# Kernel optimization log

Hardware: AMD Instinct MI355X
Metric: run time of the kernel (lower is better)

Reference implementation:

```python
import jax, jax.numpy as jnp
import numpy as np

N = 50000      # num_nodes
E = 800000     # num_edges
F = 29         # num_node_features
IN = F + 3     # in_channels after hstack with pos
H = 64         # hidden_dim
B = 50         # batch_size (num graphs)
L = 7          # num GINConv layers


def setup_inputs() -> dict:
    key = jax.random.key(0)
    ks = jax.random.split(key, 12)
    s_in = 1.0 / np.sqrt(IN)
    s_h = 1.0 / np.sqrt(H)
    return {
        "x": jax.random.normal(ks[0], (N, F), jnp.float32),
        "pos": jax.random.normal(ks[1], (N, 3), jnp.float32),
        "edge_index": jax.random.randint(ks[2], (2, E), 0, N),
        "batch": jnp.sort(jax.random.randint(ks[3], (N,), 0, B)),
        # GINConv l: MLP = Linear(in,H) -> ReLU -> Linear(H,H)
        "W1_first": jax.random.normal(ks[4], (IN, H), jnp.float32) * s_in,
        "W1_rest": jax.random.normal(ks[5], (L - 1, H, H), jnp.float32) * s_h,
        "b1": jax.random.normal(ks[6], (L, H), jnp.float32) * 0.01,
        "W2": jax.random.normal(ks[7], (L, H, H), jnp.float32) * s_h,
        "b2": jax.random.normal(ks[8], (L, H), jnp.float32) * 0.01,
        "lin_w": jax.random.normal(ks[9], (H, 1), jnp.float32) * s_h,
        "lin_b": jax.random.normal(ks[10], (1,), jnp.float32) * 0.01,
    }


def reference(x, pos, edge_index, batch, W1_first, W1_rest, b1, W2, b2, lin_w, lin_b):
    src, dst = edge_index[0], edge_index[1]
    h = jnp.concatenate([x, pos], axis=1)  # [N, IN]

    def gin_conv(h, Wa, ba, Wb, bb):
        # sum aggregation of source features at destination nodes, eps=0
        agg = jax.ops.segment_sum(h[src], dst, num_segments=N)
        z = h + agg
        z = jax.nn.relu(z @ Wa + ba)
        return z @ Wb + bb

    h = jax.nn.relu(gin_conv(h, W1_first, b1[0], W2[0], b2[0]))
    for l in range(1, L):
        h = gin_conv(h, W1_rest[l - 1], b1[l], W2[l], b2[l])
        if l < L - 1:  # no activation after last conv (jk=None)
            h = jax.nn.relu(h)

    # global mean pool per graph
    sums = jax.ops.segment_sum(h, batch, num_segments=B)            # [B, H]
    counts = jax.ops.segment_sum(jnp.ones((N,), h.dtype), batch, num_segments=B)
    pooled = sums / jnp.maximum(counts, 1.0)[:, None]

    return pooled @ lin_w + lin_b  # [B, 1]
```

## Files before the change

### kernel.cpp

```cpp
#include <hip/hip_runtime.h>
#include <stdint.h>

#define NF 29
#define HD 64
#define NL 7
#define LDW 72
#define NCHUNK 256
#define BSH 8
#define PER_M (64 * LDW)
#define TILE 32

typedef __attribute__((ext_vector_type(8))) __bf16 bf16x8;
typedef __attribute__((ext_vector_type(4))) float floatx4;
typedef int int32x4 __attribute__((ext_vector_type(4)));
typedef float f32x4v __attribute__((ext_vector_type(4)));

extern "C" __device__ f32x4v llvm_amdgcn_raw_buffer_load_fp32x4(
    int32x4 srsrc, int voffset, int soffset, int cachepolicy)
    __asm("llvm.amdgcn.raw.buffer.load.v4f32");

__device__ __forceinline__ int32x4 make_srd(const void* p) {
    unsigned long long a = (unsigned long long)p;
    int32x4 r;
    r.x = (int)(a & 0xFFFFFFFFull);
    r.y = (int)(a >> 32);
    r.z = -1;
    r.w = 0x00020000;
    return r;
}
__device__ __forceinline__ uint4 bload16_sc0(int32x4 srd, int voff) {
    f32x4v v = llvm_amdgcn_raw_buffer_load_fp32x4(srd, voff, 0, 1 );
    union { f32x4v f; uint4 u; } c;
    c.f = v;
    return c.u;
}

__device__ __forceinline__ unsigned short f2bf(float x) {
    unsigned u = __float_as_uint(x);
    unsigned r = (u + 0x7fffu + ((u >> 16) & 1u)) >> 16;
    return (unsigned short)r;
}
__device__ __forceinline__ unsigned pack_bf2(float x, float y) {
    return (unsigned)f2bf(x) | ((unsigned)f2bf(y) << 16);
}
__device__ __forceinline__ float bflo(uint32_t u) { return __uint_as_float(u << 16); }
__device__ __forceinline__ float bfhi(uint32_t u) { return __uint_as_float(u & 0xffff0000u); }
__device__ __forceinline__ float bf2f(unsigned short s) {
    return __uint_as_float((uint32_t)s << 16);
}

__global__ void front_kernel(const float* __restrict__ x, const float* __restrict__ pos,
                             unsigned short* __restrict__ h0,
                             const float* __restrict__ W1f, const float* __restrict__ W1r,
                             const float* __restrict__ W2, unsigned short* __restrict__ wpk,
                             const int* __restrict__ dst, int E, int chunk,
                             int* __restrict__ bcnt, int* __restrict__ bsum,
                             float* __restrict__ pool, int N, int B) {
    __shared__ int hist[256];
    const int H0B = (N * 4 + 255) / 256;
    const int WPB = (NL * 2 * PER_M + 255) / 256;
    int blk = blockIdx.x;
    if (blk < H0B) {
        int t = blk * 256 + threadIdx.x;
        if (t < N * 4) {
            int n = t >> 2, q = t & 3;
            const float* xr = x + (size_t)n * NF;
            float f[8];
            if (q < 3) {
                #pragma unroll
                for (int i = 0; i < 8; ++i) f[i] = xr[q * 8 + i];
            } else {
                #pragma unroll
                for (int i = 0; i < 5; ++i) f[i] = xr[24 + i];
                f[5] = pos[n * 3 + 0]; f[6] = pos[n * 3 + 1]; f[7] = pos[n * 3 + 2];
            }
            uint4 pk;
            pk.x = pack_bf2(f[0], f[1]); pk.y = pack_bf2(f[2], f[3]);
            pk.z = pack_bf2(f[4], f[5]); pk.w = pack_bf2(f[6], f[7]);
            ((uint4*)h0)[t] = pk;
        }
    } else if (blk < H0B + WPB) {
        int bw = blk - H0B;
        if (bw == 0) {
            for (int i = threadIdx.x; i < B * HD; i += 256) pool[i] = 0.f;
        }
        int t = bw * 256 + threadIdx.x;
        if (t < NL * 2 * PER_M) {
            int l = t / (2 * PER_M);
            int r = t - l * 2 * PER_M;
            int m = r / PER_M;
            int q = r - m * PER_M;
            int j = q / LDW, k = q - j * LDW;
            float v = 0.f;
            if (m == 0) {
                int ind = (l == 0) ? 32 : 64;
                if (k < ind) v = (l == 0) ? W1f[k * 64 + j]
                                          : W1r[(size_t)(l - 1) * 4096 + (size_t)k * 64 + j];
            } else {
                if (k < 64) v = W2[(size_t)l * 4096 + (size_t)k * 64 + j];
            }
            wpk[t] = f2bf(v);
        }
    } else {
        int c = blk - H0B - WPB;
        int tid = threadIdx.x;
        hist[tid] = 0;
        __syncthreads();
        int lo = c * chunk, hi = min(E, lo + chunk);
        for (int e = lo + tid; e < hi; e += 256) atomicAdd(&hist[dst[e] >> BSH], 1);
        __syncthreads();
        bcnt[c * 256 + tid] = hist[tid];
        if (hist[tid]) atomicAdd(&bsum[tid], hist[tid]);
    }
}

__global__ void bucket_off_kernel(const int* __restrict__ bcnt, const int* __restrict__ bsum,
                                  int* __restrict__ boffT) {
    __shared__ int red[256];
    __shared__ int s[256];
    int b = blockIdx.x, t = threadIdx.x;
    red[t] = (t < b) ? bsum[t] : 0;
    int c = bcnt[t * 256 + b];
    __syncthreads();
    #pragma unroll
    for (int off = 128; off > 0; off >>= 1) {
        if (t < off) red[t] += red[t + off];
        __syncthreads();
    }
    int bstart_b = red[0];
    s[t] = c;
    __syncthreads();
    for (int off = 1; off < 256; off <<= 1) {
        int v = (t >= off) ? s[t - off] : 0;
        __syncthreads();
        s[t] += v;
        __syncthreads();
    }
    int excl = s[t] - c;
    boffT[t * 256 + b] = bstart_b + excl;
}

__global__ void bucket_scatter_kernel(const int* __restrict__ src, const int* __restrict__ dst,
                                      int E, int chunk, const int* __restrict__ boffT,
                                      unsigned int* __restrict__ ebuf) {
    __shared__ int cur[256];
    int tid = threadIdx.x, c = blockIdx.x;
    cur[tid] = boffT[c * 256 + tid];
    __syncthreads();
    int lo = c * chunk, hi = min(E, lo + chunk);
    for (int e = lo + tid; e < hi; e += 256) {
        int d = dst[e];
        int p = atomicAdd(&cur[d >> BSH], 1);
        ebuf[p] = (unsigned int)src[e] | ((unsigned int)(d & 255) << 16);
    }
}

__global__ void final_scatter_kernel(const unsigned int* __restrict__ ebuf,
                                     const int* __restrict__ bsum,
                                     int* __restrict__ rowptr,
                                     unsigned short* __restrict__ colsrc, int N, int E) {
    __shared__ int red[256];
    __shared__ int cnt[256];
    __shared__ int cur[256];
    __shared__ int s[256];
    int b = blockIdx.x, t = threadIdx.x;
    red[t] = (t < b) ? bsum[t] : 0;
    cnt[t] = 0;
    __syncthreads();
    #pragma unroll
    for (int off = 128; off > 0; off >>= 1) {
        if (t < off) red[t] += red[t + off];
        __syncthreads();
    }
    int lo = red[0];
    int hi = lo + bsum[b];
    if (b == 0 && t == 0) rowptr[N] = E;
    for (int e = lo + t; e < hi; e += 256) atomicAdd(&cnt[ebuf[e] >> 16], 1);
    __syncthreads();
    int c = cnt[t];
    s[t] = c;
    __syncthreads();
    for (int off = 1; off < 256; off <<= 1) {
        int v = (t >= off) ? s[t - off] : 0;
        __syncthreads();
        s[t] += v;
        __syncthreads();
    }
    int base = lo + s[t] - c;
    int node = (b << BSH) + t;
    if (node < N) rowptr[node] = base;
    cur[t] = base;
    __syncthreads();
    for (int e = lo + t; e < hi; e += 256) {
        unsigned int ed = ebuf[e];
        int p = atomicAdd(&cur[ed >> 16], 1);
        colsrc[p] = (unsigned short)(ed & 0xffffu);
    }
}

template<int IND, bool RELU_OUT, bool LAST>
__global__ __launch_bounds__(256, 8)
void gin_layer_kernel(const unsigned short* __restrict__ hin,
                      const int* __restrict__ rowptr, const unsigned short* __restrict__ colsrc,
                      const unsigned short* __restrict__ wAT, const unsigned short* __restrict__ wBT,
                      const float* __restrict__ ba, const float* __restrict__ bb,
                      unsigned short* __restrict__ hout,
                      const int* __restrict__ batch, float* __restrict__ pool,
                      int N)
{
    __shared__ __align__(16) unsigned short zbuf[TILE * LDW];
    __shared__ __align__(16) unsigned short t1buf[TILE * LDW];

    const int tid = threadIdx.x;
    const int lane = tid & 63;
    const int w = tid >> 6;
    const int tile0 = blockIdx.x * TILE;

    const int32x4 srd = make_srd(hin);
    const int g = lane >> 3;
    const int j = lane & 7;
    const int node = tile0 + w * 8 + g;

    int rp;
    {
        int idx = tile0 + w * 8 + (lane < 9 ? lane : 8);
        if (idx > N) idx = N;
        rp = rowptr[idx];
    }
    int e0 = __shfl(rp, g);
    int e1 = __shfl(rp, g + 1);
    if (node >= N) { e0 = 0; e1 = 0; }

    float acc[8] = {0.f, 0.f, 0.f, 0.f, 0.f, 0.f, 0.f, 0.f};
    auto addrow = [&](uint4 u) {
        acc[0] += bflo(u.x); acc[1] += bfhi(u.x);
        acc[2] += bflo(u.y); acc[3] += bfhi(u.y);
        acc[4] += bflo(u.z); acc[5] += bfhi(u.z);
        acc[6] += bflo(u.w); acc[7] += bfhi(u.w);
    };

    if constexpr (IND == 64) {
        const int f4 = lane & 7;
        if (node < N) addrow(bload16_sc0(srd, node * 128 + f4 * 16));
        int e = e0;
        int idxv = (e + j < e1) ? (int)colsrc[e + j] : 0;
        for (; e + 7 < e1; e += 8) {
            int en = e + 8;
            int idx_next = (en + j < e1) ? (int)colsrc[en + j] : 0;
            int s[8];
            #pragma unroll
            for (int q = 0; q < 8; ++q) s[q] = __shfl(idxv, g * 8 + q);
            uint4 u[8];
            #pragma unroll
            for (int q = 0; q < 8; ++q) u[q] = bload16_sc0(srd, s[q] * 128 + f4 * 16);
            #pragma unroll
            for (int q = 0; q < 8; ++q) addrow(u[q]);
            idxv = idx_next;
        }
        {
            int rem = e1 - e;
            #pragma unroll
            for (int q = 0; q < 8; ++q) {
                if (q < rem) {
                    int s = __shfl(idxv, g * 8 + q);
                    addrow(bload16_sc0(srd, s * 128 + f4 * 16));
                }
            }
        }
        uint4 pk;
        pk.x = pack_bf2(acc[0], acc[1]); pk.y = pack_bf2(acc[2], acc[3]);
        pk.z = pack_bf2(acc[4], acc[5]); pk.w = pack_bf2(acc[6], acc[7]);
        *(uint4*)&zbuf[(w * 8 + g) * LDW + f4 * 8] = pk;
    } else {
        const int p = (lane >> 2) & 1;
        const int f4 = lane & 3;
        if (node < N && p == 0) addrow(bload16_sc0(srd, node * 64 + f4 * 16));
        int e = e0 + p;
        for (; e + 7 < e1; e += 8) {
            int s0 = colsrc[e], s1 = colsrc[e + 2], s2 = colsrc[e + 4], s3 = colsrc[e + 6];
            uint4 u0 = bload16_sc0(srd, s0 * 64 + f4 * 16);
            uint4 u1 = bload16_sc0(srd, s1 * 64 + f4 * 16);
            uint4 u2 = bload16_sc0(srd, s2 * 64 + f4 * 16);
            uint4 u3 = bload16_sc0(srd, s3 * 64 + f4 * 16);
            addrow(u0); addrow(u1); addrow(u2); addrow(u3);
        }
        while (e < e1) { addrow(bload16_sc0(srd, (int)colsrc[e] * 64 + f4 * 16)); e += 2; }
        #pragma unroll
        for (int i = 0; i < 8; ++i) acc[i] += __shfl_xor(acc[i], 4);
        if (p == 0) {
            uint4 pk;
            pk.x = pack_bf2(acc[0], acc[1]); pk.y = pack_bf2(acc[2], acc[3]);
            pk.z = pack_bf2(acc[4], acc[5]); pk.w = pack_bf2(acc[6], acc[7]);
            *(uint4*)&zbuf[(w * 8 + g) * LDW + f4 * 8] = pk;
        }
    }
    __syncthreads();

    const int n0 = lane & 15, quad = lane >> 4;
    const int stripe = w & 1, jhalf = w >> 1;
    const int row0 = stripe * 16;
    const int jt0 = jhalf * 2, jt1 = jhalf * 2 + 1;

    floatx4 c0, c1;
    {
        float b0v = ba[jt0 * 16 + n0], b1v = ba[jt1 * 16 + n0];
        c0 = (floatx4){b0v, b0v, b0v, b0v};
        c1 = (floatx4){b1v, b1v, b1v, b1v};
    }
    #pragma unroll
    for (int kk = 0; kk < IND / 32; ++kk) {
        bf16x8 a   = *(const bf16x8*)&zbuf[(row0 + n0) * LDW + kk * 32 + quad * 8];
        bf16x8 br0 = *(const bf16x8*)&wAT[(jt0 * 16 + n0) * LDW + kk * 32 + quad * 8];
        bf16x8 br1 = *(const bf16x8*)&wAT[(jt1 * 16 + n0) * LDW + kk * 32 + quad * 8];
        c0 = __builtin_amdgcn_mfma_f32_16x16x32_bf16(a, br0, c0, 0, 0, 0);
        c1 = __builtin_amdgcn_mfma_f32_16x16x32_bf16(a, br1, c1, 0, 0, 0);
    }
    #pragma unroll
    for (int r = 0; r < 4; ++r) {
        int row = row0 + quad * 4 + r;
        t1buf[row * LDW + jt0 * 16 + n0] = f2bf(fmaxf(c0[r], 0.f));
        t1buf[row * LDW + jt1 * 16 + n0] = f2bf(fmaxf(c1[r], 0.f));
    }
    __syncthreads();

    {
        float b0v = bb[jt0 * 16 + n0], b1v = bb[jt1 * 16 + n0];
        c0 = (floatx4){b0v, b0v, b0v, b0v};
        c1 = (floatx4){b1v, b1v, b1v, b1v};
    }
    #pragma unroll
    for (int kk = 0; kk < 2; ++kk) {
        bf16x8 a   = *(const bf16x8*)&t1buf[(row0 + n0) * LDW + kk * 32 + quad * 8];
        bf16x8 br0 = *(const bf16x8*)&wBT[(jt0 * 16 + n0) * LDW + kk * 32 + quad * 8];
        bf16x8 br1 = *(const bf16x8*)&wBT[(jt1 * 16 + n0) * LDW + kk * 32 + quad * 8];
        c0 = __builtin_amdgcn_mfma_f32_16x16x32_bf16(a, br0, c0, 0, 0, 0);
        c1 = __builtin_amdgcn_mfma_f32_16x16x32_bf16(a, br1, c1, 0, 0, 0);
    }
    #pragma unroll
    for (int r = 0; r < 4; ++r) {
        int row = row0 + quad * 4 + r;
        float v0 = c0[r], v1 = c1[r];
        if (RELU_OUT) { v0 = fmaxf(v0, 0.f); v1 = fmaxf(v1, 0.f); }
        zbuf[row * LDW + jt0 * 16 + n0] = f2bf(v0);
        zbuf[row * LDW + jt1 * 16 + n0] = f2bf(v1);
    }
    __syncthreads();

    if constexpr (!LAST) {
        int nl = tid >> 3, c4 = tid & 7;
        int nodeo = tile0 + nl;
        if (nodeo < N) {
            uint4 v = *(const uint4*)&zbuf[nl * LDW + c4 * 8];
            ((uint4*)hout)[(size_t)nodeo * 8 + c4] = v;
        }
    } else {
        int nl0 = w * 8;
        int bvec = 0;
        if (lane < 8) {
            int idx = tile0 + nl0 + lane;
            bvec = batch[idx < N ? idx : (N - 1)];
        }
        int bsel = -1;
        float run = 0.f;
        for (int i = 0; i < 8; ++i) {
            int nodeo = tile0 + nl0 + i;
            if (nodeo >= N) break;
            int b = __shfl(bvec, i);
            float v = bf2f(zbuf[(nl0 + i) * LDW + lane]);
            if (b != bsel) {
                if (bsel >= 0) atomicAdd(&pool[bsel * HD + lane], run);
                bsel = b; run = 0.f;
            }
            run += v;
        }
        if (bsel >= 0) atomicAdd(&pool[bsel * HD + lane], run);
    }
}

__global__ void final_kernel(const float* __restrict__ pool, const int* __restrict__ batch,
                             const float* __restrict__ lin_w, const float* __restrict__ lin_b,
                             float* __restrict__ out, int B, int N) {
    int b = blockIdx.x;
    int lane = threadIdx.x;
    int lo = 0, hi = N;
    while (lo < hi) { int m = (lo + hi) >> 1; if (batch[m] < b) lo = m + 1; else hi = m; }
    int lb = lo;
    lo = 0; hi = N;
    while (lo < hi) { int m = (lo + hi) >> 1; if (batch[m] <= b) lo = m + 1; else hi = m; }
    float c = fmaxf((float)(lo - lb), 1.f);
    float v = pool[b * HD + lane] / c * lin_w[lane];
    for (int off = 32; off > 0; off >>= 1) v += __shfl_down(v, off);
    if (lane == 0) out[b] = v + lin_b[0];
}

extern "C" void kernel_launch(void* const* d_in, const int* in_sizes, int n_in,
                              void* d_out, int out_size, void* d_ws, size_t ws_size,
                              hipStream_t stream)
{
    const float* x   = (const float*)d_in[0];
    const float* pos = (const float*)d_in[1];
    const int*  eidx = (const int*)d_in[2];
    const int* batch = (const int*)d_in[3];
    const float* W1f = (const float*)d_in[4];
    const float* W1r = (const float*)d_in[5];
    const float* b1  = (const float*)d_in[6];
    const float* W2  = (const float*)d_in[7];
    const float* b2  = (const float*)d_in[8];
    const float* lw  = (const float*)d_in[9];
    const float* lb  = (const float*)d_in[10];

    int N = in_sizes[3];
    int E = in_sizes[2] / 2;
    int B = out_size;
    const int* src = eidx;
    const int* dst = eidx + E;

    char* ws = (char*)d_ws;
    size_t off = 0;
    auto alloc = [&](size_t bytes) -> void* {
        void* p = ws + off;
        off += (bytes + 255) & ~(size_t)255;
        return p;
    };
    unsigned short* bufA = (unsigned short*)alloc((size_t)N * HD * 2);
    unsigned short* bufB = (unsigned short*)alloc((size_t)N * HD * 2);
    int*   rowptr = (int*)  alloc((size_t)(N + 1) * 4);
    unsigned short* colsrc = (unsigned short*)alloc((size_t)E * 2);
    unsigned int* ebuf = (unsigned int*)alloc((size_t)E * 4);
    float* pool   = (float*)alloc((size_t)B * HD * 4);
    int*   bcnt   = (int*)  alloc((size_t)NCHUNK * 256 * 4);
    int*   boffT  = (int*)  alloc((size_t)NCHUNK * 256 * 4);
    int*   bsum   = (int*)  alloc(256 * 4);
    unsigned short* wpk = (unsigned short*)alloc((size_t)NL * 2 * PER_M * 2);

    hipMemsetAsync(bsum, 0, 256 * 4, stream);

    int nbuk = (N + 255) >> BSH;
    int chunk = (E + NCHUNK - 1) / NCHUNK;

    const int H0B = (N * 4 + 255) / 256;
    const int WPB = (NL * 2 * PER_M + 255) / 256;
    front_kernel<<<H0B + WPB + NCHUNK, 256, 0, stream>>>(
        x, pos, bufA, W1f, W1r, W2, wpk, dst, E, chunk, bcnt, bsum, pool, N, B);
    bucket_off_kernel<<<nbuk, 256, 0, stream>>>(bcnt, bsum, boffT);
    bucket_scatter_kernel<<<NCHUNK, 256, 0, stream>>>(src, dst, E, chunk, boffT, ebuf);
    final_scatter_kernel<<<nbuk, 256, 0, stream>>>(ebuf, bsum, rowptr, colsrc, N, E);

    const int gblocks = (N + TILE - 1) / TILE;
    gin_layer_kernel<32, true, false><<<gblocks, 256, 0, stream>>>(
        bufA, rowptr, colsrc, wpk + 0 * PER_M, wpk + 1 * PER_M, b1, b2, bufB,
        nullptr, nullptr, N);
    unsigned short* cur_in = bufB;
    unsigned short* cur_out = bufA;
    for (int l = 1; l < NL; ++l) {
        const unsigned short* wa = wpk + (size_t)(2 * l + 0) * PER_M;
        const unsigned short* wb = wpk + (size_t)(2 * l + 1) * PER_M;
        const float* ba = b1 + l * HD;
        const float* bb = b2 + l * HD;
        if (l < NL - 1) {
            gin_layer_kernel<HD, true, false><<<gblocks, 256, 0, stream>>>(
                cur_in, rowptr, colsrc, wa, wb, ba, bb, cur_out, nullptr, nullptr, N);
            unsigned short* tmp = cur_in; cur_in = cur_out; cur_out = tmp;
        } else {
            gin_layer_kernel<HD, false, true><<<gblocks, 256, 0, stream>>>(
                cur_in, rowptr, colsrc, wa, wb, ba, bb, nullptr, batch, pool, N);
        }
    }
    final_kernel<<<B, 64, 0, stream>>>(pool, batch, lw, lb, (float*)d_out, B, N);
}
```

Baseline: 240.1 us.

## Add 16-node-tile GIN layer kernel with 16 lanes per node for hidden layers

Adds a new kernel for the 64-wide hidden layers that processes 16 nodes per block instead of 32. Each node's edges are gathered by 16 lanes split into two edge-parity halves, which are combined with a shuffle. The MLP runs as a single 16x16 MFMA tile per wave. The aim is to double the number of blocks and the memory-level parallelism for the irregular neighbour gather, which should hide latency better. In exchange, the weight loads and block overhead are paid once per 16 nodes instead of per 32, and part of the MFMA work is wasted on a smaller tile.

```diff
diff --git a/kernel.cpp b/kernel.cpp
--- a/kernel.cpp
+++ b/kernel.cpp
@@ -218,7 +218,6 @@
 
     const int32x4 srd = make_srd(hin);
     const int g = lane >> 3;
-    const int j = lane & 7;
     const int node = tile0 + w * 8 + g;
 
     int rp;
@@ -239,39 +238,7 @@
         acc[6] += bflo(u.w); acc[7] += bfhi(u.w);
     };
 
-    if constexpr (IND == 64) {
-        const int f4 = lane & 7;
-        if (node < N) addrow(bload16_sc0(srd, node * 128 + f4 * 16));
-        int e = e0;
-        int idxv = (e + j < e1) ? (int)colsrc[e + j] : 0;
-        for (; e + 7 < e1; e += 8) {
-            int en = e + 8;
-            int idx_next = (en + j < e1) ? (int)colsrc[en + j] : 0;
-            int s[8];
-            #pragma unroll
-            for (int q = 0; q < 8; ++q) s[q] = __shfl(idxv, g * 8 + q);
-            uint4 u[8];
-            #pragma unroll
-            for (int q = 0; q < 8; ++q) u[q] = bload16_sc0(srd, s[q] * 128 + f4 * 16);
-            #pragma unroll
-            for (int q = 0; q < 8; ++q) addrow(u[q]);
-            idxv = idx_next;
-        }
-        {
-            int rem = e1 - e;
-            #pragma unroll
-            for (int q = 0; q < 8; ++q) {
-                if (q < rem) {
-                    int s = __shfl(idxv, g * 8 + q);
-                    addrow(bload16_sc0(srd, s * 128 + f4 * 16));
-                }
-            }
-        }
-        uint4 pk;
-        pk.x = pack_bf2(acc[0], acc[1]); pk.y = pack_bf2(acc[2], acc[3]);
-        pk.z = pack_bf2(acc[4], acc[5]); pk.w = pack_bf2(acc[6], acc[7]);
-        *(uint4*)&zbuf[(w * 8 + g) * LDW + f4 * 8] = pk;
-    } else {
+    {
         const int p = (lane >> 2) & 1;
         const int f4 = lane & 3;
         if (node < N && p == 0) addrow(bload16_sc0(srd, node * 64 + f4 * 16));
@@ -374,6 +341,153 @@
             run += v;
         }
         if (bsel >= 0) atomicAdd(&pool[bsel * HD + lane], run);
+    }
+}
+
+template<bool RELU_OUT, bool LAST>
+__global__ __launch_bounds__(256, 8)
+void gin_layer16_kernel(const unsigned short* __restrict__ hin,
+                        const int* __restrict__ rowptr, const unsigned short* __restrict__ colsrc,
+                        const unsigned short* __restrict__ wAT, const unsigned short* __restrict__ wBT,
+                        const float* __restrict__ ba, const float* __restrict__ bb,
+                        unsigned short* __restrict__ hout,
+                        const int* __restrict__ batch, float* __restrict__ pool,
+                        int N)
+{
+    __shared__ __align__(16) unsigned short zbuf[16 * LDW];
+    __shared__ __align__(16) unsigned short t1buf[16 * LDW];
+
+    const int tid = threadIdx.x;
+    const int lane = tid & 63;
+    const int w = tid >> 6;
+    const int tile0 = blockIdx.x * 16;
+
+    const int32x4 srd = make_srd(hin);
+    const int g = lane >> 4;
+    const int u = lane & 15;
+    const int p = u >> 3;
+    const int f4 = u & 7;
+    const int node = tile0 + w * 4 + g;
+
+    int rp;
+    {
+        int idx = tile0 + w * 4 + (lane < 5 ? lane : 4);
+        if (idx > N) idx = N;
+        rp = rowptr[idx];
+    }
+    int e0 = __shfl(rp, g);
+    int e1 = __shfl(rp, g + 1);
+    if (node >= N) { e0 = 0; e1 = 0; }
+
+    float acc[8] = {0.f, 0.f, 0.f, 0.f, 0.f, 0.f, 0.f, 0.f};
+    auto addrow = [&](uint4 uu) {
+        acc[0] += bflo(uu.x); acc[1] += bfhi(uu.x);
+        acc[2] += bflo(uu.y); acc[3] += bfhi(uu.y);
+        acc[4] += bflo(uu.z); acc[5] += bfhi(uu.z);
+        acc[6] += bflo(uu.w); acc[7] += bfhi(uu.w);
+    };
+
+    if (node < N && p == 0) addrow(bload16_sc0(srd, node * 128 + f4 * 16));
+
+    int eb = e0;
+    int idxv = (eb + u < e1) ? (int)colsrc[eb + u] : 0;
+    for (; eb + 15 < e1; eb += 16) {
+        int ebn = eb + 16;
+        int idx_next = (ebn + u < e1) ? (int)colsrc[ebn + u] : 0;
+        int s[8];
+        #pragma unroll
+        for (int q = 0; q < 8; ++q) s[q] = __shfl(idxv, g * 16 + 2 * q + p);
+        uint4 uu[8];
+        #pragma unroll
+        for (int q = 0; q < 8; ++q) uu[q] = bload16_sc0(srd, s[q] * 128 + f4 * 16);
+        #pragma unroll
+        for (int q = 0; q < 8; ++q) addrow(uu[q]);
+        idxv = idx_next;
+    }
+    {
+        int rem = e1 - eb;
+        #pragma unroll
+        for (int q = 0; q < 8; ++q) {
+            int s = __shfl(idxv, g * 16 + 2 * q + p);
+            if (2 * q + p < rem) addrow(bload16_sc0(srd, s * 128 + f4 * 16));
+        }
+    }
+    #pragma unroll
+    for (int i = 0; i < 8; ++i) acc[i] += __shfl_xor(acc[i], 8);
+    if (p == 0) {
+        uint4 pk;
+        pk.x = pack_bf2(acc[0], acc[1]); pk.y = pack_bf2(acc[2], acc[3]);
+        pk.z = pack_bf2(acc[4], acc[5]); pk.w = pack_bf2(acc[6], acc[7]);
+        *(uint4*)&zbuf[(w * 4 + g) * LDW + f4 * 8] = pk;
+    }
+    __syncthreads();
+
+    const int n0 = lane & 15, quad = lane >> 4;
+    floatx4 c0;
+    {
+        float b0v = ba[w * 16 + n0];
+        c0 = (floatx4){b0v, b0v, b0v, b0v};
+    }
+    #pragma unroll
+    for (int kk = 0; kk < 2; ++kk) {
+        bf16x8 a  = *(const bf16x8*)&zbuf[n0 * LDW + kk * 32 + quad * 8];
+        bf16x8 br = *(const bf16x8*)&wAT[(w * 16 + n0) * LDW + kk * 32 + quad * 8];
+        c0 = __builtin_amdgcn_mfma_f32_16x16x32_bf16(a, br, c0, 0, 0, 0);
+    }
+    #pragma unroll
+    for (int r = 0; r < 4; ++r) {
+        t1buf[(quad * 4 + r) * LDW + w * 16 + n0] = f2bf(fmaxf(c0[r], 0.f));
+    }
+    __syncthreads();
+
+    {
+        float b0v = bb[w * 16 + n0];
+        c0 = (floatx4){b0v, b0v, b0v, b0v};
+    }
+    #pragma unroll
+    for (int kk = 0; kk < 2; ++kk) {
+        bf16x8 a  = *(const bf16x8*)&t1buf[n0 * LDW + kk * 32 + quad * 8];
+        bf16x8 br = *(const bf16x8*)&wBT[(w * 16 + n0) * LDW + kk * 32 + quad * 8];
+        c0 = __builtin_amdgcn_mfma_f32_16x16x32_bf16(a, br, c0, 0, 0, 0);
+    }
+    #pragma unroll
+    for (int r = 0; r < 4; ++r) {
+        float v0 = c0[r];
+        if (RELU_OUT) v0 = fmaxf(v0, 0.f);
+        zbuf[(quad * 4 + r) * LDW + w * 16 + n0] = f2bf(v0);
+    }
+    __syncthreads();
+
+    if constexpr (!LAST) {
+        int nl = tid >> 4, c2 = tid & 15;
+        int nodeo = tile0 + nl;
+        if (nodeo < N) {
+            uint2 v = *(const uint2*)&zbuf[nl * LDW + c2 * 4];
+            ((uint2*)hout)[(size_t)nodeo * 16 + c2] = v;
+        }
+    } else {
+        if (w < 2) {
+            int nl0 = w * 8;
+            int bvec = 0;
+            if (lane < 8) {
+                int idx = tile0 + nl0 + lane;
+                bvec = batch[idx < N ? idx : (N - 1)];
+            }
+            int bsel = -1;
+            float run = 0.f;
+            for (int i = 0; i < 8; ++i) {
+                int nodeo = tile0 + nl0 + i;
+                if (nodeo >= N) break;
+                int b = __shfl(bvec, i);
+                float v = bf2f(zbuf[(nl0 + i) * LDW + lane]);
+                if (b != bsel) {
+                    if (bsel >= 0) atomicAdd(&pool[bsel * HD + lane], run);
+                    bsel = b; run = 0.f;
+                }
+                run += v;
+            }
+            if (bsel >= 0) atomicAdd(&pool[bsel * HD + lane], run);
+        }
     }
 }
 
@@ -446,8 +560,9 @@
     bucket_scatter_kernel<<<NCHUNK, 256, 0, stream>>>(src, dst, E, chunk, boffT, ebuf);
     final_scatter_kernel<<<nbuk, 256, 0, stream>>>(ebuf, bsum, rowptr, colsrc, N, E);
 
-    const int gblocks = (N + TILE - 1) / TILE;
-    gin_layer_kernel<32, true, false><<<gblocks, 256, 0, stream>>>(
+    const int gblocks32 = (N + TILE - 1) / TILE;
+    const int gblocks16 = (N + 15) / 16;
+    gin_layer_kernel<32, true, false><<<gblocks32, 256, 0, stream>>>(
         bufA, rowptr, colsrc, wpk + 0 * PER_M, wpk + 1 * PER_M, b1, b2, bufB,
         nullptr, nullptr, N);
     unsigned short* cur_in = bufB;
@@ -458,11 +573,11 @@
         const float* ba = b1 + l * HD;
         const float* bb = b2 + l * HD;
         if (l < NL - 1) {
-            gin_layer_kernel<HD, true, false><<<gblocks, 256, 0, stream>>>(
+            gin_layer16_kernel<true, false><<<gblocks16, 256, 0, stream>>>(
                 cur_in, rowptr, colsrc, wa, wb, ba, bb, cur_out, nullptr, nullptr, N);
             unsigned short* tmp = cur_in; cur_in = cur_out; cur_out = tmp;
         } else {
-            gin_layer_kernel<HD, false, true><<<gblocks, 256, 0, stream>>>(
+            gin_layer16_kernel<false, true><<<gblocks16, 256, 0, stream>>>(
                 cur_in, rowptr, colsrc, wa, wb, ba, bb, nullptr, batch, pool, N);
         }
     }
```

Measured after the change: 250.3 us. 4.2% more time.

## Sort nodes by in-degree so each tile processes similar-degree rows

Applied to the files above, without the earlier changes.

Builds a degree-sorted node permutation via a per-bucket degree histogram, a prefix offset kernel and a permutation scatter, then has every GIN layer process nodes in permuted order. The goal is to balance gather work across the 8 node-groups in a wave so lanes don't idle waiting on the highest-degree node. The cost is two extra preprocessing launches and loss of spatial locality: output writes and self-row reads become scattered, and the final pooling gets more fragmented batch runs and so more atomics.

```diff
diff --git a/kernel.cpp b/kernel.cpp
--- a/kernel.cpp
+++ b/kernel.cpp
@@ -55,7 +55,8 @@
                              const float* __restrict__ W2, unsigned short* __restrict__ wpk,
                              const int* __restrict__ dst, int E, int chunk,
                              int* __restrict__ bcnt, int* __restrict__ bsum,
-                             float* __restrict__ pool, int N, int B) {
+                             float* __restrict__ pool, int* __restrict__ dsum,
+                             int N, int B) {
     __shared__ int hist[256];
     const int H0B = (N * 4 + 255) / 256;
     const int WPB = (NL * 2 * PER_M + 255) / 256;
@@ -83,6 +84,7 @@
         int bw = blk - H0B;
         if (bw == 0) {
             for (int i = threadIdx.x; i < B * HD; i += 256) pool[i] = 0.f;
+            dsum[threadIdx.x] = 0;
         }
         int t = bw * 256 + threadIdx.x;
         if (t < NL * 2 * PER_M) {
@@ -158,14 +160,18 @@
 __global__ void final_scatter_kernel(const unsigned int* __restrict__ ebuf,
                                      const int* __restrict__ bsum,
                                      int* __restrict__ rowptr,
-                                     unsigned short* __restrict__ colsrc, int N, int E) {
+                                     unsigned short* __restrict__ colsrc,
+                                     int* __restrict__ degarr, int* __restrict__ dcnt,
+                                     int* __restrict__ dsum, int N, int E) {
     __shared__ int red[256];
     __shared__ int cnt[256];
     __shared__ int cur[256];
     __shared__ int s[256];
+    __shared__ int dh[256];
     int b = blockIdx.x, t = threadIdx.x;
     red[t] = (t < b) ? bsum[t] : 0;
     cnt[t] = 0;
+    dh[t] = 0;
     __syncthreads();
     #pragma unroll
     for (int off = 128; off > 0; off >>= 1) {
@@ -188,7 +194,11 @@
     }
     int base = lo + s[t] - c;
     int node = (b << BSH) + t;
-    if (node < N) rowptr[node] = base;
+    if (node < N) {
+        rowptr[node] = base;
+        degarr[node] = c;
+        atomicAdd(&dh[min(c, 255)], 1);
+    }
     cur[t] = base;
     __syncthreads();
     for (int e = lo + t; e < hi; e += 256) {
@@ -196,12 +206,56 @@
         int p = atomicAdd(&cur[ed >> 16], 1);
         colsrc[p] = (unsigned short)(ed & 0xffffu);
     }
+    __syncthreads();
+    dcnt[b * 256 + t] = dh[t];
+    if (dh[t]) atomicAdd(&dsum[t], dh[t]);
+}
+
+__global__ void deg_off_kernel(const int* __restrict__ dcnt, const int* __restrict__ dsum,
+                               int* __restrict__ doffT, int nchunk) {
+    __shared__ int red[256];
+    __shared__ int s[256];
+    int b = blockIdx.x, t = threadIdx.x;
+    red[t] = (t < b) ? dsum[t] : 0;
+    int c = (t < nchunk) ? dcnt[t * 256 + b] : 0;
+    __syncthreads();
+    #pragma unroll
+    for (int off = 128; off > 0; off >>= 1) {
+        if (t < off) red[t] += red[t + off];
+        __syncthreads();
+    }
+    int dstart_b = red[0];
+    s[t] = c;
+    __syncthreads();
+    for (int off = 1; off < 256; off <<= 1) {
+        int v = (t >= off) ? s[t - off] : 0;
+        __syncthreads();
+        s[t] += v;
+        __syncthreads();
+    }
+    int excl = s[t] - c;
+    doffT[t * 256 + b] = dstart_b + excl;
+}
+
+__global__ void perm_kernel(const int* __restrict__ degarr, const int* __restrict__ doffT,
+                            int* __restrict__ perm, int N) {
+    __shared__ int cur[256];
+    int b = blockIdx.x, t = threadIdx.x;
+    cur[t] = doffT[b * 256 + t];
+    __syncthreads();
+    int node = (b << BSH) + t;
+    if (node < N) {
+        int d = min(degarr[node], 255);
+        int pos = atomicAdd(&cur[d], 1);
+        perm[pos] = node;
+    }
 }
 
 template<int IND, bool RELU_OUT, bool LAST>
 __global__ __launch_bounds__(256, 8)
 void gin_layer_kernel(const unsigned short* __restrict__ hin,
                       const int* __restrict__ rowptr, const unsigned short* __restrict__ colsrc,
+                      const int* __restrict__ perm,
                       const unsigned short* __restrict__ wAT, const unsigned short* __restrict__ wBT,
                       const float* __restrict__ ba, const float* __restrict__ bb,
                       unsigned short* __restrict__ hout,
@@ -218,18 +272,14 @@
 
     const int32x4 srd = make_srd(hin);
     const int g = lane >> 3;
-    const int j = lane & 7;
-    const int node = tile0 + w * 8 + g;
-
-    int rp;
-    {
-        int idx = tile0 + w * 8 + (lane < 9 ? lane : 8);
-        if (idx > N) idx = N;
-        rp = rowptr[idx];
-    }
-    int e0 = __shfl(rp, g);
-    int e1 = __shfl(rp, g + 1);
-    if (node >= N) { e0 = 0; e1 = 0; }
+    const int node_p = tile0 + w * 8 + g;
+
+    int node = 0, e0 = 0, e1 = 0;
+    if (node_p < N) {
+        node = perm[node_p];
+        e0 = rowptr[node];
+        e1 = rowptr[node + 1];
+    }
 
     float acc[8] = {0.f, 0.f, 0.f, 0.f, 0.f, 0.f, 0.f, 0.f};
     auto addrow = [&](uint4 u) {
@@ -240,8 +290,9 @@
     };
 
     if constexpr (IND == 64) {
+        const int j = lane & 7;
         const int f4 = lane & 7;
-        if (node < N) addrow(bload16_sc0(srd, node * 128 + f4 * 16));
+        if (node_p < N) addrow(bload16_sc0(srd, node * 128 + f4 * 16));
         int e = e0;
         int idxv = (e + j < e1) ? (int)colsrc[e + j] : 0;
         for (; e + 7 < e1; e += 8) {
@@ -274,7 +325,7 @@
     } else {
         const int p = (lane >> 2) & 1;
         const int f4 = lane & 3;
-        if (node < N && p == 0) addrow(bload16_sc0(srd, node * 64 + f4 * 16));
+        if (node_p < N && p == 0) addrow(bload16_sc0(srd, node * 64 + f4 * 16));
         int e = e0 + p;
         for (; e + 7 < e1; e += 8) {
             int s0 = colsrc[e], s1 = colsrc[e + 2], s2 = colsrc[e + 4], s3 = colsrc[e + 6];
@@ -348,8 +399,9 @@
 
     if constexpr (!LAST) {
         int nl = tid >> 3, c4 = tid & 7;
-        int nodeo = tile0 + nl;
-        if (nodeo < N) {
+        int nodeo_p = tile0 + nl;
+        if (nodeo_p < N) {
+            int nodeo = perm[nodeo_p];
             uint4 v = *(const uint4*)&zbuf[nl * LDW + c4 * 8];
             ((uint4*)hout)[(size_t)nodeo * 8 + c4] = v;
         }
@@ -357,14 +409,14 @@
         int nl0 = w * 8;
         int bvec = 0;
         if (lane < 8) {
-            int idx = tile0 + nl0 + lane;
-            bvec = batch[idx < N ? idx : (N - 1)];
+            int idxp = tile0 + nl0 + lane;
+            bvec = batch[perm[idxp < N ? idxp : (N - 1)]];
         }
         int bsel = -1;
         float run = 0.f;
         for (int i = 0; i < 8; ++i) {
-            int nodeo = tile0 + nl0 + i;
-            if (nodeo >= N) break;
+            int nodeo_p = tile0 + nl0 + i;
+            if (nodeo_p >= N) break;
             int b = __shfl(bvec, i);
             float v = bf2f(zbuf[(nl0 + i) * LDW + lane]);
             if (b != bsel) {
@@ -431,6 +483,11 @@
     int*   bcnt   = (int*)  alloc((size_t)NCHUNK * 256 * 4);
     int*   boffT  = (int*)  alloc((size_t)NCHUNK * 256 * 4);
     int*   bsum   = (int*)  alloc(256 * 4);
+    int*   degarr = (int*)  alloc((size_t)N * 4);
+    int*   dcnt   = (int*)  alloc((size_t)256 * 256 * 4);
+    int*   doffT2 = (int*)  alloc((size_t)256 * 256 * 4);
+    int*   dsum   = (int*)  alloc(256 * 4);
+    int*   perm   = (int*)  alloc((size_t)N * 4);
     unsigned short* wpk = (unsigned short*)alloc((size_t)NL * 2 * PER_M * 2);
 
     hipMemsetAsync(bsum, 0, 256 * 4, stream);
@@ -441,14 +498,17 @@
     const int H0B = (N * 4 + 255) / 256;
     const int WPB = (NL * 2 * PER_M + 255) / 256;
     front_kernel<<<H0B + WPB + NCHUNK, 256, 0, stream>>>(
-        x, pos, bufA, W1f, W1r, W2, wpk, dst, E, chunk, bcnt, bsum, pool, N, B);
+        x, pos, bufA, W1f, W1r, W2, wpk, dst, E, chunk, bcnt, bsum, pool, dsum, N, B);
     bucket_off_kernel<<<nbuk, 256, 0, stream>>>(bcnt, bsum, boffT);
     bucket_scatter_kernel<<<NCHUNK, 256, 0, stream>>>(src, dst, E, chunk, boffT, ebuf);
-    final_scatter_kernel<<<nbuk, 256, 0, stream>>>(ebuf, bsum, rowptr, colsrc, N, E);
+    final_scatter_kernel<<<nbuk, 256, 0, stream>>>(ebuf, bsum, rowptr, colsrc,
+                                                   degarr, dcnt, dsum, N, E);
+    deg_off_kernel<<<256, 256, 0, stream>>>(dcnt, dsum, doffT2, nbuk);
+    perm_kernel<<<nbuk, 256, 0, stream>>>(degarr, doffT2, perm, N);
 
     const int gblocks = (N + TILE - 1) / TILE;
     gin_layer_kernel<32, true, false><<<gblocks, 256, 0, stream>>>(
-        bufA, rowptr, colsrc, wpk + 0 * PER_M, wpk + 1 * PER_M, b1, b2, bufB,
+        bufA, rowptr, colsrc, perm, wpk + 0 * PER_M, wpk + 1 * PER_M, b1, b2, bufB,
         nullptr, nullptr, N);
     unsigned short* cur_in = bufB;
     unsigned short* cur_out = bufA;
@@ -459,11 +519,11 @@
         const float* bb = b2 + l * HD;
         if (l < NL - 1) {
             gin_layer_kernel<HD, true, false><<<gblocks, 256, 0, stream>>>(
-                cur_in, rowptr, colsrc, wa, wb, ba, bb, cur_out, nullptr, nullptr, N);
+                cur_in, rowptr, colsrc, perm, wa, wb, ba, bb, cur_out, nullptr, nullptr, N);
             unsigned short* tmp = cur_in; cur_in = cur_out; cur_out = tmp;
         } else {
             gin_layer_kernel<HD, false, true><<<gblocks, 256, 0, stream>>>(
-                cur_in, rowptr, colsrc, wa, wb, ba, bb, nullptr, batch, pool, N);
+                cur_in, rowptr, colsrc, perm, wa, wb, ba, bb, nullptr, batch, pool, N);
         }
     }
     final_kernel<<<B, 64, 0, stream>>>(pool, batch, lw, lb, (float*)d_out, B, N);
```

New measurement: 251.8 us. 4.9% more time.

## Split hidden features into two 32-column tables and gather each half separately

Applied to the files above, without the earlier changes.

Hidden activations are stored as two separate N×32 bf16 tables (columns 0-31 and 32-63) instead of one N×64 table. The 64-wide aggregation now runs the 32-wide gather routine twice, once per half table, so each pass touches a smaller working set that fits better in cache. The cost is walking the edge list and colsrc indices twice per layer, and the 8-edge shuffle-prefetched gather path for IND=64 is removed.

```diff
diff --git a/kernel.cpp b/kernel.cpp
--- a/kernel.cpp
+++ b/kernel.cpp
@@ -200,11 +200,12 @@
 
 template<int IND, bool RELU_OUT, bool LAST>
 __global__ __launch_bounds__(256, 8)
-void gin_layer_kernel(const unsigned short* __restrict__ hin,
+void gin_layer_kernel(const unsigned short* __restrict__ hinA,
+                      const unsigned short* __restrict__ hinB,
                       const int* __restrict__ rowptr, const unsigned short* __restrict__ colsrc,
                       const unsigned short* __restrict__ wAT, const unsigned short* __restrict__ wBT,
                       const float* __restrict__ ba, const float* __restrict__ bb,
-                      unsigned short* __restrict__ hout,
+                      unsigned short* __restrict__ houtA, unsigned short* __restrict__ houtB,
                       const int* __restrict__ batch, float* __restrict__ pool,
                       int N)
 {
@@ -216,10 +217,10 @@
     const int w = tid >> 6;
     const int tile0 = blockIdx.x * TILE;
 
-    const int32x4 srd = make_srd(hin);
     const int g = lane >> 3;
-    const int j = lane & 7;
     const int node = tile0 + w * 8 + g;
+    const int p = (lane >> 2) & 1;
+    const int f4 = lane & 3;
 
     int rp;
     {
@@ -231,49 +232,17 @@
     int e1 = __shfl(rp, g + 1);
     if (node >= N) { e0 = 0; e1 = 0; }
 
-    float acc[8] = {0.f, 0.f, 0.f, 0.f, 0.f, 0.f, 0.f, 0.f};
+    float acc[8];
     auto addrow = [&](uint4 u) {
         acc[0] += bflo(u.x); acc[1] += bfhi(u.x);
         acc[2] += bflo(u.y); acc[3] += bfhi(u.y);
         acc[4] += bflo(u.z); acc[5] += bfhi(u.z);
         acc[6] += bflo(u.w); acc[7] += bfhi(u.w);
     };
-
-    if constexpr (IND == 64) {
-        const int f4 = lane & 7;
-        if (node < N) addrow(bload16_sc0(srd, node * 128 + f4 * 16));
-        int e = e0;
-        int idxv = (e + j < e1) ? (int)colsrc[e + j] : 0;
-        for (; e + 7 < e1; e += 8) {
-            int en = e + 8;
-            int idx_next = (en + j < e1) ? (int)colsrc[en + j] : 0;
-            int s[8];
-            #pragma unroll
-            for (int q = 0; q < 8; ++q) s[q] = __shfl(idxv, g * 8 + q);
-            uint4 u[8];
-            #pragma unroll
-            for (int q = 0; q < 8; ++q) u[q] = bload16_sc0(srd, s[q] * 128 + f4 * 16);
-            #pragma unroll
-            for (int q = 0; q < 8; ++q) addrow(u[q]);
-            idxv = idx_next;
-        }
-        {
-            int rem = e1 - e;
-            #pragma unroll
-            for (int q = 0; q < 8; ++q) {
-                if (q < rem) {
-                    int s = __shfl(idxv, g * 8 + q);
-                    addrow(bload16_sc0(srd, s * 128 + f4 * 16));
-                }
-            }
-        }
-        uint4 pk;
-        pk.x = pack_bf2(acc[0], acc[1]); pk.y = pack_bf2(acc[2], acc[3]);
-        pk.z = pack_bf2(acc[4], acc[5]); pk.w = pack_bf2(acc[6], acc[7]);
-        *(uint4*)&zbuf[(w * 8 + g) * LDW + f4 * 8] = pk;
-    } else {
-        const int p = (lane >> 2) & 1;
-        const int f4 = lane & 3;
+    auto gather_half = [&](const unsigned short* tbl, int colbase) {
+        const int32x4 srd = make_srd(tbl);
+        #pragma unroll
+        for (int i = 0; i < 8; ++i) acc[i] = 0.f;
         if (node < N && p == 0) addrow(bload16_sc0(srd, node * 64 + f4 * 16));
         int e = e0 + p;
         for (; e + 7 < e1; e += 8) {
@@ -291,8 +260,13 @@
             uint4 pk;
             pk.x = pack_bf2(acc[0], acc[1]); pk.y = pack_bf2(acc[2], acc[3]);
             pk.z = pack_bf2(acc[4], acc[5]); pk.w = pack_bf2(acc[6], acc[7]);
-            *(uint4*)&zbuf[(w * 8 + g) * LDW + f4 * 8] = pk;
-        }
+            *(uint4*)&zbuf[(w * 8 + g) * LDW + colbase + f4 * 8] = pk;
+        }
+    };
+
+    gather_half(hinA, 0);
+    if constexpr (IND == 64) {
+        gather_half(hinB, 32);
     }
     __syncthreads();
 
@@ -351,7 +325,8 @@
         int nodeo = tile0 + nl;
         if (nodeo < N) {
             uint4 v = *(const uint4*)&zbuf[nl * LDW + c4 * 8];
-            ((uint4*)hout)[(size_t)nodeo * 8 + c4] = v;
+            if (c4 < 4) ((uint4*)houtA)[(size_t)nodeo * 4 + c4] = v;
+            else        ((uint4*)houtB)[(size_t)nodeo * 4 + (c4 - 4)] = v;
         }
     } else {
         int nl0 = w * 8;
@@ -446,12 +421,18 @@
     bucket_scatter_kernel<<<NCHUNK, 256, 0, stream>>>(src, dst, E, chunk, boffT, ebuf);
     final_scatter_kernel<<<nbuk, 256, 0, stream>>>(ebuf, bsum, rowptr, colsrc, N, E);
 
+    const size_t nhalf = (size_t)N * 32;
+    unsigned short* A0 = bufA;
+    unsigned short* B_A = bufB;
+    unsigned short* B_B = bufB + nhalf;
+    unsigned short* A_A = bufA;
+    unsigned short* A_B = bufA + nhalf;
+
     const int gblocks = (N + TILE - 1) / TILE;
     gin_layer_kernel<32, true, false><<<gblocks, 256, 0, stream>>>(
-        bufA, rowptr, colsrc, wpk + 0 * PER_M, wpk + 1 * PER_M, b1, b2, bufB,
-        nullptr, nullptr, N);
-    unsigned short* cur_in = bufB;
-    unsigned short* cur_out = bufA;
+        A0, nullptr, rowptr, colsrc, wpk + 0 * PER_M, wpk + 1 * PER_M, b1, b2,
+        B_A, B_B, nullptr, nullptr, N);
+    unsigned short *ciA = B_A, *ciB = B_B, *coA = A_A, *coB = A_B;
     for (int l = 1; l < NL; ++l) {
         const unsigned short* wa = wpk + (size_t)(2 * l + 0) * PER_M;
         const unsigned short* wb = wpk + (size_t)(2 * l + 1) * PER_M;
@@ -459,11 +440,13 @@
         const float* bb = b2 + l * HD;
         if (l < NL - 1) {
             gin_layer_kernel<HD, true, false><<<gblocks, 256, 0, stream>>>(
-                cur_in, rowptr, colsrc, wa, wb, ba, bb, cur_out, nullptr, nullptr, N);
-            unsigned short* tmp = cur_in; cur_in = cur_out; cur_out = tmp;
+                ciA, ciB, rowptr, colsrc, wa, wb, ba, bb, coA, coB, nullptr, nullptr, N);
+            unsigned short* t;
+            t = ciA; ciA = coA; coA = t;
+            t = ciB; ciB = coB; coB = t;
         } else {
             gin_layer_kernel<HD, false, true><<<gblocks, 256, 0, stream>>>(
-                cur_in, rowptr, colsrc, wa, wb, ba, bb, nullptr, batch, pool, N);
+                ciA, ciB, rowptr, colsrc, wa, wb, ba, bb, nullptr, nullptr, batch, pool, N);
         }
     }
     final_kernel<<<B, 64, 0, stream>>>(pool, batch, lw, lb, (float*)d_out, B, N);
```

Result: slower. 260.9 us (+8.6%).
